# Kernel optimization log

Measured on AMD Instinct MI355X. Metric: run time of the kernel, lower is better.

Reference implementation:

```python
import jax, jax.numpy as jnp
import numpy as np
from jax import lax

C, H, W = 256, 512, 512


def setup_inputs() -> dict:
    key = jax.random.key(0)
    x = jax.random.normal(key, (C, H, W), dtype=jnp.float32)
    return {"x": x}


def reference(x):
    # Original torch code mutates x in-place: top pooling first (reverse
    # cummax along H, i.e. max over rows below), then left pooling on the
    # ALREADY top-pooled tensor (reverse cummax along W). `top` and `left`
    # alias the same storage, so out = t + t = 2 * t.
    t = lax.cummax(x, axis=1, reverse=True)   # top pool: propagate maxima upward
    t = lax.cummax(t, axis=2, reverse=True)   # left pool: propagate maxima leftward
    return t + t
```

## Files before the change

### kernel.cpp

```cpp
#include <hip/hip_runtime.h>
#include <math.h>

constexpr int C     = 256;
constexpr int H     = 512;
constexpr int W     = 512;
constexpr int RPW   = 4;
constexpr int BATCH = 8 * RPW;

__device__ __forceinline__ float4 fmax4(float4 x, float4 y) {
    return make_float4(fmaxf(x.x, y.x), fmaxf(x.y, y.y),
                       fmaxf(x.z, y.z), fmaxf(x.w, y.w));
}

__global__ __launch_bounds__(512)
void tlc_kernel(const float* __restrict__ x, float* __restrict__ out) {
    const int tid  = threadIdx.x;
    const int g    = tid >> 6;
    const int lane = tid & 63;
    const int c    = blockIdx.x;
    const int col  = lane * 8;

    __shared__ float4 ltotA[2][8][64], ltotB[2][8][64];
    __shared__ float4 gcolA[2][64],    gcolB[2][64];

    const float* __restrict__ xc = x   + (size_t)c * H * W;
    float*       __restrict__ oc = out + (size_t)c * H * W;

    const int s1  = min(lane + 1, 63), s2  = min(lane + 2, 63);
    const int s4  = min(lane + 4, 63), s8  = min(lane + 8, 63);
    const int s16 = min(lane + 16, 63), s32 = min(lane + 32, 63);

    if (g == 0) {
        const float4 ninf = make_float4(-INFINITY, -INFINITY, -INFINITY, -INFINITY);
        gcolA[0][lane] = ninf;
        gcolB[0][lane] = ninf;
    }

    int   buf = 0;
    int   rowbase = (H - BATCH) + RPW * g;
    float4 curA[RPW], curB[RPW], nxtA[RPW], nxtB[RPW];

    #pragma unroll
    for (int r = 0; r < RPW; ++r) {
        const float* p = xc + (size_t)(rowbase + r) * W + col;
        curA[r] = *(const float4*)p;
        curB[r] = *(const float4*)(p + 4);
    }

    for (int hb = H - BATCH; hb >= 0; hb -= BATCH, rowbase -= BATCH) {
        if (hb >= BATCH) {
            #pragma unroll
            for (int r = 0; r < RPW; ++r) {
                const float* p = xc + (size_t)(rowbase - BATCH + r) * W + col;
                nxtA[r] = *(const float4*)p;
                nxtB[r] = *(const float4*)(p + 4);
            }
        }

        float4 pA[RPW], pB[RPW];
        pA[RPW - 1] = curA[RPW - 1];
        pB[RPW - 1] = curB[RPW - 1];
        #pragma unroll
        for (int r = RPW - 2; r >= 0; --r) {
            pA[r] = fmax4(curA[r], pA[r + 1]);
            pB[r] = fmax4(curB[r], pB[r + 1]);
        }

        ltotA[buf][g][lane] = pA[0];
        ltotB[buf][g][lane] = pB[0];
        __syncthreads();

        float4 mA = gcolA[buf][lane];
        float4 mB = gcolB[buf][lane];
        for (int gg = g + 1; gg < 8; ++gg) {
            mA = fmax4(mA, ltotA[buf][gg][lane]);
            mB = fmax4(mB, ltotB[buf][gg][lane]);
        }

        if (g == 0) {
            gcolA[buf ^ 1][lane] = fmax4(pA[0], mA);
            gcolB[buf ^ 1][lane] = fmax4(pB[0], mB);
        }

        #pragma unroll
        for (int r = 0; r < RPW; ++r) {
            const float4 vA = fmax4(pA[r], mA);
            const float4 vB = fmax4(pB[r], mB);

            const float t7 = vB.w;
            const float t6 = fmaxf(vB.z, t7);
            const float t5 = fmaxf(vB.y, t6);
            const float t4 = fmaxf(vB.x, t5);
            const float t3 = fmaxf(vA.w, t4);
            const float t2 = fmaxf(vA.z, t3);
            const float t1 = fmaxf(vA.y, t2);
            const float t0 = fmaxf(vA.x, t1);

            float e = __shfl(t0, s1);
            e = (lane == 63) ? -INFINITY : e;
            e = fmaxf(e, __shfl(e, s1));
            e = fmaxf(e, __shfl(e, s2));
            e = fmaxf(e, __shfl(e, s4));
            e = fmaxf(e, __shfl(e, s8));
            e = fmaxf(e, __shfl(e, s16));
            e = fmaxf(e, __shfl(e, s32));

            float4 oA, oB;
            oA.x = 2.0f * fmaxf(t0, e);
            oA.y = 2.0f * fmaxf(t1, e);
            oA.z = 2.0f * fmaxf(t2, e);
            oA.w = 2.0f * fmaxf(t3, e);
            oB.x = 2.0f * fmaxf(t4, e);
            oB.y = 2.0f * fmaxf(t5, e);
            oB.z = 2.0f * fmaxf(t6, e);
            oB.w = 2.0f * fmaxf(t7, e);

            float* q = oc + (size_t)(rowbase + r) * W + col;
            *(float4*)q       = oA;
            *(float4*)(q + 4) = oB;
        }

        #pragma unroll
        for (int r = 0; r < RPW; ++r) {
            curA[r] = nxtA[r];
            curB[r] = nxtB[r];
        }
        buf ^= 1;
    }
}

extern "C" void kernel_launch(void* const* d_in, const int* in_sizes, int n_in,
                              void* d_out, int out_size, void* d_ws, size_t ws_size,
                              hipStream_t stream) {
    const float* x   = (const float*)d_in[0];
    float*       out = (float*)d_out;
    tlc_kernel<<<dim3(C), dim3(512), 0, stream>>>(x, out);
}
```

Measured before the change: 114.0 us.

## Scan along W before the column scan and double rows per wave

The leftward scan along W (register chain plus wave shuffles) now runs on each raw row before the cross-wave column reduction. The final pass then only takes a max with the column carry from the rows below and scales by two. This is valid because suffix maxima along the two axes commute: both orders give the max over the lower-right rectangle. The shuffle work now sits ahead of the barrier, so it can overlap with other waves, and the post-sync critical path gets shorter. Rows per wave go from 4 to 8, which halves the loop trips and barriers but roughly doubles register pressure for the prefetch buffers.

```diff
diff --git a/kernel.cpp b/kernel.cpp
--- a/kernel.cpp
+++ b/kernel.cpp
@@ -4,7 +4,7 @@
 constexpr int C     = 256;
 constexpr int H     = 512;
 constexpr int W     = 512;
-constexpr int RPW   = 4;
+constexpr int RPW   = 8;
 constexpr int BATCH = 8 * RPW;
 
 __device__ __forceinline__ float4 fmax4(float4 x, float4 y) {
@@ -26,8 +26,8 @@
     const float* __restrict__ xc = x   + (size_t)c * H * W;
     float*       __restrict__ oc = out + (size_t)c * H * W;
 
-    const int s1  = min(lane + 1, 63), s2  = min(lane + 2, 63);
-    const int s4  = min(lane + 4, 63), s8  = min(lane + 8, 63);
+    const int s1  = min(lane + 1, 63),  s2  = min(lane + 2, 63);
+    const int s4  = min(lane + 4, 63),  s8  = min(lane + 8, 63);
     const int s16 = min(lane + 16, 63), s32 = min(lane + 32, 63);
 
     if (g == 0) {
@@ -36,15 +36,15 @@
         gcolB[0][lane] = ninf;
     }
 
-    int   buf = 0;
-    int   rowbase = (H - BATCH) + RPW * g;
-    float4 curA[RPW], curB[RPW], nxtA[RPW], nxtB[RPW];
+    int buf = 0;
+    int rowbase = (H - BATCH) + RPW * g;
+    float4 cA[RPW], cB[RPW], nA[RPW], nB[RPW];
 
     #pragma unroll
     for (int r = 0; r < RPW; ++r) {
         const float* p = xc + (size_t)(rowbase + r) * W + col;
-        curA[r] = *(const float4*)p;
-        curB[r] = *(const float4*)(p + 4);
+        cA[r] = *(const float4*)p;
+        cB[r] = *(const float4*)(p + 4);
     }
 
     for (int hb = H - BATCH; hb >= 0; hb -= BATCH, rowbase -= BATCH) {
@@ -52,22 +52,46 @@
             #pragma unroll
             for (int r = 0; r < RPW; ++r) {
                 const float* p = xc + (size_t)(rowbase - BATCH + r) * W + col;
-                nxtA[r] = *(const float4*)p;
-                nxtB[r] = *(const float4*)(p + 4);
+                nA[r] = *(const float4*)p;
+                nB[r] = *(const float4*)(p + 4);
             }
         }
 
-        float4 pA[RPW], pB[RPW];
-        pA[RPW - 1] = curA[RPW - 1];
-        pB[RPW - 1] = curB[RPW - 1];
+        #pragma unroll
+        for (int r = 0; r < RPW; ++r) {
+            const float4 a = cA[r], b = cB[r];
+            const float t7 = b.w;
+            const float t6 = fmaxf(b.z, t7);
+            const float t5 = fmaxf(b.y, t6);
+            const float t4 = fmaxf(b.x, t5);
+            const float t3 = fmaxf(a.w, t4);
+            const float t2 = fmaxf(a.z, t3);
+            const float t1 = fmaxf(a.y, t2);
+            const float t0 = fmaxf(a.x, t1);
+
+            float e = __shfl(t0, s1);
+            e = (lane == 63) ? -INFINITY : e;
+            e = fmaxf(e, __shfl(e, s1));
+            e = fmaxf(e, __shfl(e, s2));
+            e = fmaxf(e, __shfl(e, s4));
+            e = fmaxf(e, __shfl(e, s8));
+            e = fmaxf(e, __shfl(e, s16));
+            e = fmaxf(e, __shfl(e, s32));
+
+            cA[r] = make_float4(fmaxf(t0, e), fmaxf(t1, e),
+                                fmaxf(t2, e), fmaxf(t3, e));
+            cB[r] = make_float4(fmaxf(t4, e), fmaxf(t5, e),
+                                fmaxf(t6, e), fmaxf(t7, e));
+        }
+
         #pragma unroll
         for (int r = RPW - 2; r >= 0; --r) {
-            pA[r] = fmax4(curA[r], pA[r + 1]);
-            pB[r] = fmax4(curB[r], pB[r + 1]);
+            cA[r] = fmax4(cA[r], cA[r + 1]);
+            cB[r] = fmax4(cB[r], cB[r + 1]);
         }
 
-        ltotA[buf][g][lane] = pA[0];
-        ltotB[buf][g][lane] = pB[0];
+        ltotA[buf][g][lane] = cA[0];
+        ltotB[buf][g][lane] = cB[0];
         __syncthreads();
 
         float4 mA = gcolA[buf][lane];
@@ -78,52 +102,25 @@
         }
 
         if (g == 0) {
-            gcolA[buf ^ 1][lane] = fmax4(pA[0], mA);
-            gcolB[buf ^ 1][lane] = fmax4(pB[0], mB);
+            gcolA[buf ^ 1][lane] = fmax4(cA[0], mA);
+            gcolB[buf ^ 1][lane] = fmax4(cB[0], mB);
         }
 
         #pragma unroll
         for (int r = 0; r < RPW; ++r) {
-            const float4 vA = fmax4(pA[r], mA);
-            const float4 vB = fmax4(pB[r], mB);
-
-            const float t7 = vB.w;
-            const float t6 = fmaxf(vB.z, t7);
-            const float t5 = fmaxf(vB.y, t6);
-            const float t4 = fmaxf(vB.x, t5);
-            const float t3 = fmaxf(vA.w, t4);
-            const float t2 = fmaxf(vA.z, t3);
-            const float t1 = fmaxf(vA.y, t2);
-            const float t0 = fmaxf(vA.x, t1);
-
-            float e = __shfl(t0, s1);
-            e = (lane == 63) ? -INFINITY : e;
-            e = fmaxf(e, __shfl(e, s1));
-            e = fmaxf(e, __shfl(e, s2));
-            e = fmaxf(e, __shfl(e, s4));
-            e = fmaxf(e, __shfl(e, s8));
-            e = fmaxf(e, __shfl(e, s16));
-            e = fmaxf(e, __shfl(e, s32));
-
-            float4 oA, oB;
-            oA.x = 2.0f * fmaxf(t0, e);
-            oA.y = 2.0f * fmaxf(t1, e);
-            oA.z = 2.0f * fmaxf(t2, e);
-            oA.w = 2.0f * fmaxf(t3, e);
-            oB.x = 2.0f * fmaxf(t4, e);
-            oB.y = 2.0f * fmaxf(t5, e);
-            oB.z = 2.0f * fmaxf(t6, e);
-            oB.w = 2.0f * fmaxf(t7, e);
-
+            const float4 oA = fmax4(cA[r], mA);
+            const float4 oB = fmax4(cB[r], mB);
             float* q = oc + (size_t)(rowbase + r) * W + col;
-            *(float4*)q       = oA;
-            *(float4*)(q + 4) = oB;
+            *(float4*)q       = make_float4(2.0f * oA.x, 2.0f * oA.y,
+                                            2.0f * oA.z, 2.0f * oA.w);
+            *(float4*)(q + 4) = make_float4(2.0f * oB.x, 2.0f * oB.y,
+                                            2.0f * oB.z, 2.0f * oB.w);
         }
 
         #pragma unroll
         for (int r = 0; r < RPW; ++r) {
-            curA[r] = nxtA[r];
-            curB[r] = nxtB[r];
+            cA[r] = nA[r];
+            cB[r] = nB[r];
         }
         buf ^= 1;
     }
```

Measured after the change: 119.6 us. 4.9% more time.
